# Optimization experiments

Hardware: AMD Instinct MI355X
Metric: run time of the kernel (lower is better)

Reference implementation:

```python
import jax, jax.numpy as jnp
import numpy as np

D_MODEL = 1024
NUM_HEADS = 16
HEAD_SIZE = D_MODEL // NUM_HEADS
THETA = 10000.0
MAX_SEQ_LEN = 4096


def _rope_tables():
    # (max_seq_len, head_size//2) cos/sin tables, matching RotaryPositionalEmbedding
    k = jnp.arange(HEAD_SIZE // 2, dtype=jnp.float32)
    inv_freq = 1.0 / (THETA ** (2.0 * k / HEAD_SIZE))
    pos = jnp.arange(MAX_SEQ_LEN, dtype=jnp.float32)
    ang = pos[:, None] * inv_freq[None, :]
    return jnp.cos(ang), jnp.sin(ang)


def _apply_rope(x, cos, sin):
    # x: (b, h, s, d); cos/sin: (s, d//2) -> broadcast over (b, h)
    x1 = x[..., ::2]
    x2 = x[..., 1::2]
    out_even = x1 * cos - x2 * sin
    out_odd = x2 * cos + x1 * sin
    # re-interleave pairs back to (..., d)
    return jnp.stack([out_even, out_odd], axis=-1).reshape(x.shape)


def setup_inputs() -> dict:
    key = jax.random.key(0)
    k1, k2, k3 = jax.random.split(key, 3)
    b, s = 1, 4096
    std_qkv = np.sqrt(2.0 / (D_MODEL + 3 * D_MODEL))
    std_o = np.sqrt(2.0 / (D_MODEL + D_MODEL))
    return {
        "x": jax.random.normal(k1, (b, s, D_MODEL), dtype=jnp.float32),
        "token_positions": jnp.arange(s, dtype=jnp.int32),
        "W_qkv": jax.random.normal(k2, (3 * D_MODEL, D_MODEL), dtype=jnp.float32) * std_qkv,
        "W_o": jax.random.normal(k3, (D_MODEL, D_MODEL), dtype=jnp.float32) * std_o,
    }


def reference(x, token_positions, W_qkv, W_o):
    b, s, _ = x.shape
    qkv = jnp.einsum("bsd,ed->bse", x, W_qkv)  # (b, s, 3*d_model)
    q, k, v = jnp.split(qkv, 3, axis=-1)

    def to_heads(t):
        return t.reshape(b, s, NUM_HEADS, HEAD_SIZE).transpose(0, 2, 1, 3)  # (b, h, s, hs)

    q, k, v = to_heads(q), to_heads(k), to_heads(v)

    cos_tab, sin_tab = _rope_tables()
    cos = cos_tab[token_positions]  # (s, hs//2)
    sin = sin_tab[token_positions]
    q = _apply_rope(q, cos, sin)
    k = _apply_rope(k, cos, sin)

    scale = 1.0 / jnp.sqrt(jnp.asarray(HEAD_SIZE, dtype=x.dtype))
    scores = jnp.einsum("bhqd,bhkd->bhqk", q, k) * scale  # (b, h, s, s)
    causal = jnp.tril(jnp.ones((s, s), dtype=bool))
    scores = jnp.where(causal, scores, jnp.finfo(scores.dtype).min)
    attn = jax.nn.softmax(scores, axis=-1)
    out = jnp.einsum("bhqk,bhkd->bhqd", attn, v)  # (b, h, s, hs)
    out = out.transpose(0, 2, 1, 3).reshape(b, s, D_MODEL)
    return jnp.einsum("bsd,ed->bse", out, W_o)
```

## Files before the change

### kernel.cpp

```cpp
#include <hip/hip_runtime.h>
#include <stdint.h>

typedef unsigned short u16;
typedef __attribute__((ext_vector_type(8))) short bf16x8;
typedef __attribute__((ext_vector_type(4))) float f32x4;

#define LN_THETA 9.210340371976184f
#define SLEN 4096
#define DMODEL 1024

__device__ __forceinline__ u16 f2bf(float f) {
  union { float f; unsigned u; } v; v.f = f;
  unsigned u = v.u;
  return (u16)((u + 0x7FFFu + ((u >> 16) & 1u)) >> 16);
}
__device__ __forceinline__ u16 f2bf_trunc(float f) {
  union { float f; unsigned u; } v; v.f = f;
  return (u16)(v.u >> 16);
}
__device__ __forceinline__ float bf2f(u16 b) {
  union { unsigned u; float f; } v; v.u = ((unsigned)b) << 16;
  return v.f;
}

__device__ __forceinline__ f32x4 mfma16(bf16x8 a, bf16x8 b, f32x4 c) {
  return __builtin_amdgcn_mfma_f32_16x16x32_bf16(a, b, c, 0, 0, 0);
}

__device__ __forceinline__ void async16(const u16* g, u16* l) {
  __builtin_amdgcn_global_load_lds(
      (const __attribute__((address_space(1))) unsigned int*)g,
      (__attribute__((address_space(3))) unsigned int*)l, 16, 0, 0);
}

__global__ void rope_tab_kernel(const int* __restrict__ tokpos,
                                float2* __restrict__ tab) {
  int t = blockIdx.x * 256 + threadIdx.x;
  int s = t >> 5, i = t & 31;
  float inv = expf(-(float)(2 * i) * (LN_THETA / 64.0f));
  float ang = (float)tokpos[s] * inv;
  float sn, cs;
  sincosf(ang, &sn, &cs);
  tab[t] = make_float2(cs, sn);
}

__global__ void cvt_all_kernel(const float* __restrict__ x,
                               const float* __restrict__ wqkv,
                               const float* __restrict__ wo,
                               u16* __restrict__ xb, u16* __restrict__ wqkvb,
                               u16* __restrict__ wob) {
  int i = blockIdx.x * 256 + threadIdx.x;
  const float* src;
  u16* dst;
  if (i < (1 << 20)) {
    src = x; dst = xb;
  } else if (i < (1 << 20) + (3 << 18)) {
    i -= (1 << 20); src = wqkv; dst = wqkvb;
  } else {
    i -= (1 << 20) + (3 << 18); src = wo; dst = wob;
  }
  float4 v = ((const float4*)src)[i];
  ushort4 o;
  o.x = f2bf(v.x); o.y = f2bf(v.y); o.z = f2bf(v.z); o.w = f2bf(v.w);
  ((ushort4*)dst)[i] = o;
}

__global__ __launch_bounds__(256) void gemm_qkv_kernel(
    const u16* __restrict__ A, const u16* __restrict__ B,
    u16* __restrict__ qb, u16* __restrict__ kb,
    u16* __restrict__ vbT, const float2* __restrict__ cstab) {
  const int K = 1024;
  __shared__ __align__(16) char smem[128 * 136 * 2];
  u16 (*As)[64] = (u16(*)[64])smem;
  u16 (*Bs)[64] = (u16(*)[64])(smem + 16384);
  u16 (*Ts)[136] = (u16(*)[136])smem;
  const int tid = threadIdx.x;
  const int wave = tid >> 6, lane = tid & 63;
  const int quad = lane >> 4, col = lane & 15;
  const int rowBase = blockIdx.x * 128;
  const int colBase = blockIdx.y * 128;
  const int wm = (wave >> 1) * 64, wn = (wave & 1) * 64;

  const int sr8 = lane >> 3;
  const int sseg = ((lane & 7) ^ sr8) * 8;
  const u16* gA = A + (size_t)(rowBase + wave * 8 + sr8) * K + sseg;
  const u16* gB = B + (size_t)(colBase + wave * 8 + sr8) * K + sseg;
  u16* ldsA = &As[wave * 8 + sr8][(lane & 7) * 8];
  u16* ldsB = &Bs[wave * 8 + sr8][(lane & 7) * 8];

  const int segh[2] = {((quad ^ (col & 7)) * 8), (((4 + quad) ^ (col & 7)) * 8)};

  f32x4 acc[4][4];
#pragma unroll
  for (int i = 0; i < 4; ++i)
#pragma unroll
    for (int j = 0; j < 4; ++j)
      acc[i][j] = f32x4{0.f, 0.f, 0.f, 0.f};

  for (int kk = 0; kk < K; kk += 64) {
    __syncthreads();
#pragma unroll
    for (int j = 0; j < 4; ++j) {
      async16(gA + (size_t)j * 32 * K + kk, ldsA + j * 32 * 64);
      async16(gB + (size_t)j * 32 * K + kk, ldsB + j * 32 * 64);
    }
    __syncthreads();
#pragma unroll
    for (int h = 0; h < 2; ++h) {
      bf16x8 af[4], bfr[4];
#pragma unroll
      for (int i = 0; i < 4; ++i)
        af[i] = *(const bf16x8*)&As[wm + i * 16 + col][segh[h]];
#pragma unroll
      for (int j = 0; j < 4; ++j)
        bfr[j] = *(const bf16x8*)&Bs[wn + j * 16 + col][segh[h]];
#pragma unroll
      for (int i = 0; i < 4; ++i)
#pragma unroll
        for (int j = 0; j < 4; ++j)
          acc[i][j] = mfma16(af[i], bfr[j], acc[i][j]);
    }
  }
  __syncthreads();

  const int sec = rowBase >> 10;

  if (sec < 2) {
    const float qs = (sec == 0) ? 0.125f : 1.0f;
#pragma unroll
    for (int j = 0; j < 4; ++j) {
      int sl = wn + j * 16 + col;
      int s = colBase + sl;
#pragma unroll
      for (int i = 0; i < 4; ++i) {
        int el = wm + i * 16 + quad * 4;
        int d = (rowBase + el) & 63;
        float v0 = acc[i][j][0], v1 = acc[i][j][1];
        float v2 = acc[i][j][2], v3 = acc[i][j][3];
        float2 cs0 = cstab[s * 32 + (d >> 1)];
        float2 cs1 = cstab[s * 32 + (d >> 1) + 1];
        ushort4 pk;
        pk.x = f2bf(qs * (v0 * cs0.x - v1 * cs0.y));
        pk.y = f2bf(qs * (v1 * cs0.x + v0 * cs0.y));
        pk.z = f2bf(qs * (v2 * cs1.x - v3 * cs1.y));
        pk.w = f2bf(qs * (v3 * cs1.x + v2 * cs1.y));
        *(ushort4*)&Ts[sl][el] = pk;
      }
    }
    __syncthreads();
    int sl = tid >> 1, hf = tid & 1;
    int hh = ((rowBase & 1023) >> 6) + hf;
    u16* dst = (sec == 0 ? qb : kb) + ((size_t)hh * SLEN + colBase + sl) * 64;
    const u16* srcp = &Ts[sl][hf * 64];
#pragma unroll
    for (int kq = 0; kq < 8; ++kq)
      ((int4*)dst)[kq] = ((const int4*)srcp)[kq];
  } else {
#pragma unroll
    for (int j = 0; j < 4; ++j) {
      int sl = wn + j * 16 + col;
#pragma unroll
      for (int i = 0; i < 4; ++i) {
        int el = wm + i * 16 + quad * 4;
#pragma unroll
        for (int r = 0; r < 4; ++r)
          Ts[el + r][sl] = f2bf(acc[i][j][r]);
      }
    }
    __syncthreads();
    int el = tid >> 1, sh = tid & 1;
    int e = rowBase - 2048 + el;
    int hh = e >> 6, d = e & 63;
    u16* dst = vbT + (size_t)(hh * 64 + d) * SLEN + colBase + sh * 64;
    const u16* srcp = &Ts[el][sh * 64];
#pragma unroll
    for (int kq = 0; kq < 8; ++kq)
      ((int4*)dst)[kq] = ((const int4*)srcp)[kq];
  }
}

__global__ __launch_bounds__(256) void gemm_out_kernel(
    const u16* __restrict__ A, const u16* __restrict__ B,
    float* __restrict__ outf) {
  const int K = 1024;
  __shared__ __align__(16) u16 As[128][64];
  __shared__ __align__(16) u16 Bs[64][64];
  const int tid = threadIdx.x;
  const int wave = tid >> 6, lane = tid & 63;
  const int quad = lane >> 4, col = lane & 15;
  const int rowBase = blockIdx.x * 128;
  const int colBase = blockIdx.y * 64;

  const int sr8 = lane >> 3;
  const int sseg = ((lane & 7) ^ sr8) * 8;
  const u16* gA = A + (size_t)(rowBase + wave * 8 + sr8) * K + sseg;
  const u16* gB = B + (size_t)(colBase + wave * 8 + sr8) * K + sseg;
  u16* ldsA = &As[wave * 8 + sr8][(lane & 7) * 8];
  u16* ldsB = &Bs[wave * 8 + sr8][(lane & 7) * 8];

  const int segh[2] = {((quad ^ (col & 7)) * 8), (((4 + quad) ^ (col & 7)) * 8)};

  f32x4 acc[2][4];
#pragma unroll
  for (int i = 0; i < 2; ++i)
#pragma unroll
    for (int j = 0; j < 4; ++j)
      acc[i][j] = f32x4{0.f, 0.f, 0.f, 0.f};

  for (int kk = 0; kk < K; kk += 64) {
    __syncthreads();
#pragma unroll
    for (int j = 0; j < 4; ++j)
      async16(gA + (size_t)j * 32 * K + kk, ldsA + j * 32 * 64);
#pragma unroll
    for (int j = 0; j < 2; ++j)
      async16(gB + (size_t)j * 32 * K + kk, ldsB + j * 32 * 64);
    __syncthreads();
#pragma unroll
    for (int h = 0; h < 2; ++h) {
      bf16x8 af[2], bfr[4];
#pragma unroll
      for (int i = 0; i < 2; ++i)
        af[i] = *(const bf16x8*)&As[wave * 32 + i * 16 + col][segh[h]];
#pragma unroll
      for (int j = 0; j < 4; ++j)
        bfr[j] = *(const bf16x8*)&Bs[j * 16 + col][segh[h]];
#pragma unroll
      for (int i = 0; i < 2; ++i)
#pragma unroll
        for (int j = 0; j < 4; ++j)
          acc[i][j] = mfma16(af[i], bfr[j], acc[i][j]);
    }
  }

#pragma unroll
  for (int i = 0; i < 2; ++i) {
    int r0 = rowBase + wave * 32 + i * 16 + quad * 4;
#pragma unroll
    for (int j = 0; j < 4; ++j) {
      int cc = colBase + j * 16 + col;
#pragma unroll
      for (int r = 0; r < 4; ++r)
        outf[(size_t)(r0 + r) * DMODEL + cc] = acc[i][j][r];
    }
  }
}

__global__ __launch_bounds__(128) void flash_kernel(
    const u16* __restrict__ qbuf, const u16* __restrict__ kbuf,
    const u16* __restrict__ vbT, u16* __restrict__ po,
    float* __restrict__ pl) {
  const int S = SLEN;
  const int h = blockIdx.x;
  const int y = blockIdx.y;
  int tile, c0, c1;
  if (y < 32) {
    tile = 32 + y; c0 = 0; c1 = 31;
  } else {
    int k = (y - 32) >> 1;
    if ((y - 32) & 1) { tile = 31 - k; c0 = 0; c1 = tile; }
    else { tile = 63 - k; c0 = 32; c1 = tile; }
  }
  const int id = (tile < 32) ? tile : (32 + 2 * (tile - 32) + (c0 ? 1 : 0));

  const int wave = threadIdx.x >> 6, lane = threadIdx.x & 63;
  const int quad = lane >> 4, col = lane & 15;
  const u16* Q = qbuf + (size_t)h * S * 64;
  const u16* Kh = kbuf + (size_t)h * S * 64;
  const u16* Vt = vbT + (size_t)h * 64 * S;

  __shared__ __align__(16) u16 Ks[64][64];
  __shared__ __align__(16) u16 Vs[64][64];
  __shared__ __align__(16) u16 Pld[2][2][16][72];

  const int sr = lane >> 3;
  const int sw = ((lane & 7) ^ sr) * 8;
  const int dcol = (lane & 7) * 8;
  const int segA = ((quad ^ (col & 7)) * 8);
  const int segB = (((quad ^ 4) ^ (col & 7)) * 8);

  const int qrow0 = tile * 64 + wave * 32;

  bf16x8 qf0[2], qf1[2];
#pragma unroll
  for (int i = 0; i < 2; ++i) {
    const u16* qp = &Q[(size_t)(qrow0 + i * 16 + col) * 64 + quad * 8];
    qf0[i] = *(const bf16x8*)qp;
    qf1[i] = *(const bf16x8*)(qp + 32);
  }

  const bf16x8 ones = {(short)0x3F80, (short)0x3F80, (short)0x3F80,
                       (short)0x3F80, (short)0x3F80, (short)0x3F80,
                       (short)0x3F80, (short)0x3F80};

  f32x4 o[2][4], lacc[2];
#pragma unroll
  for (int i = 0; i < 2; ++i) {
#pragma unroll
    for (int n = 0; n < 4; ++n) o[i][n] = f32x4{0.f, 0.f, 0.f, 0.f};
    lacc[i] = f32x4{0.f, 0.f, 0.f, 0.f};
  }

  for (int c = c0; c <= c1; ++c) {
    const int k0 = c * 64;
    __syncthreads();
    {
#pragma unroll
      for (int t = 0; t < 4; ++t) {
        int row = (t * 2 + wave) * 8 + sr;
        async16(Kh + (size_t)(k0 + row) * 64 + sw, &Ks[row][dcol]);
        async16(Vt + (size_t)row * S + k0 + sw, &Vs[row][dcol]);
      }
    }
    __syncthreads();

    bf16x8 kf0[4], kf1[4], vf0[4], vf1[4];
#pragma unroll
    for (int j = 0; j < 4; ++j) {
      kf0[j] = *(const bf16x8*)&Ks[16 * j + col][segA];
      kf1[j] = *(const bf16x8*)&Ks[16 * j + col][segB];
    }
#pragma unroll
    for (int n = 0; n < 4; ++n) {
      vf0[n] = *(const bf16x8*)&Vs[16 * n + col][segA];
      vf1[n] = *(const bf16x8*)&Vs[16 * n + col][segB];
    }
    const bool lastc = (c == tile);
#pragma unroll
    for (int i = 0; i < 2; ++i) {
      f32x4 s[4];
#pragma unroll
      for (int j = 0; j < 4; ++j)
        s[j] = mfma16(qf1[i], kf1[j],
                      mfma16(qf0[i], kf0[j], f32x4{0.f, 0.f, 0.f, 0.f}));
      float p[4][4];
#pragma unroll
      for (int r = 0; r < 4; ++r) {
        const int qrel = wave * 32 + i * 16 + quad * 4 + r;
#pragma unroll
        for (int j = 0; j < 4; ++j) {
          float e = __expf(s[j][r]);
          if (lastc && (16 * j + col > qrel)) e = 0.f;
          p[j][r] = e;
        }
      }
#pragma unroll
      for (int j = 0; j < 4; ++j)
#pragma unroll
        for (int r = 0; r < 4; ++r)
          Pld[wave][i][quad * 4 + r][16 * j + col] = f2bf_trunc(p[j][r]);
      bf16x8 pa0 = *(const bf16x8*)&Pld[wave][i][col][quad * 8];
      bf16x8 pa1 = *(const bf16x8*)&Pld[wave][i][col][quad * 8 + 32];
      lacc[i] = mfma16(pa1, ones, mfma16(pa0, ones, lacc[i]));
#pragma unroll
      for (int n = 0; n < 4; ++n)
        o[i][n] = mfma16(pa1, vf1[n], mfma16(pa0, vf0[n], o[i][n]));
    }
  }

  u16* pob = po + (((size_t)h * 96 + id) * 64) * 64;
  float* plb = pl + ((size_t)h * 96 + id) * 64;
#pragma unroll
  for (int i = 0; i < 2; ++i) {
#pragma unroll
    for (int r = 0; r < 4; ++r) {
      int rowl = wave * 32 + i * 16 + quad * 4 + r;
      u16* dst = pob + (size_t)rowl * 64 + col;
#pragma unroll
      for (int n = 0; n < 4; ++n) dst[16 * n] = f2bf(o[i][n][r]);
      if (col == 0) plb[rowl] = lacc[i][r];
    }
  }
}

__global__ __launch_bounds__(256) void reduce_kernel(
    const u16* __restrict__ po, const float* __restrict__ pl,
    u16* __restrict__ attn) {
  const int h = blockIdx.x, tile = blockIdx.y;
  const int tid = threadIdx.x;
  const int row = tid >> 2, dg = (tid & 3) * 16;
  int id0, ns;
  if (tile < 32) { id0 = tile; ns = 1; }
  else { id0 = 32 + 2 * (tile - 32); ns = 2; }

  float acc[16];
#pragma unroll
  for (int q = 0; q < 16; ++q) acc[q] = 0.f;
  float l = 0.f;
  for (int s = 0; s < ns; ++s) {
    const size_t base = ((size_t)h * 96 + id0 + s) * 64;
    const u16* p = po + (base + row) * 64 + dg;
    l += pl[base + row];
#pragma unroll
    for (int q = 0; q < 16; ++q) acc[q] += bf2f(p[q]);
  }
  float inv = 1.0f / l;
  u16* dst = attn + (size_t)(tile * 64 + row) * DMODEL + h * 64 + dg;
  ushort4 o0, o1, o2, o3;
  o0.x = f2bf(acc[0] * inv);  o0.y = f2bf(acc[1] * inv);
  o0.z = f2bf(acc[2] * inv);  o0.w = f2bf(acc[3] * inv);
  o1.x = f2bf(acc[4] * inv);  o1.y = f2bf(acc[5] * inv);
  o1.z = f2bf(acc[6] * inv);  o1.w = f2bf(acc[7] * inv);
  o2.x = f2bf(acc[8] * inv);  o2.y = f2bf(acc[9] * inv);
  o2.z = f2bf(acc[10] * inv); o2.w = f2bf(acc[11] * inv);
  o3.x = f2bf(acc[12] * inv); o3.y = f2bf(acc[13] * inv);
  o3.z = f2bf(acc[14] * inv); o3.w = f2bf(acc[15] * inv);
  ((ushort4*)dst)[0] = o0; ((ushort4*)dst)[1] = o1;
  ((ushort4*)dst)[2] = o2; ((ushort4*)dst)[3] = o3;
}

extern "C" void kernel_launch(void* const* d_in, const int* in_sizes, int n_in,
                              void* d_out, int out_size, void* d_ws,
                              size_t ws_size, hipStream_t stream) {
  const float* x = (const float*)d_in[0];
  const int* tokpos = (const int*)d_in[1];
  const float* wqkv = (const float*)d_in[2];
  const float* wo = (const float*)d_in[3];
  float* out = (float*)d_out;

  char* ws = (char*)d_ws;
  u16* xb    = (u16*)(ws);
  u16* wqkvb = (u16*)(ws + ((size_t)8 << 20));
  u16* wob   = (u16*)(ws + ((size_t)14 << 20));
  u16* qb    = (u16*)(ws + ((size_t)16 << 20));
  u16* kb    = (u16*)(ws + ((size_t)24 << 20));
  u16* vbT   = (u16*)(ws + ((size_t)32 << 20));
  u16* attn  = (u16*)(ws + ((size_t)40 << 20));
  float2* cstab = (float2*)(ws + ((size_t)48 << 20));
  u16* po    = (u16*)(ws);
  float* pl  = (float*)(ws + ((size_t)13 << 20));

  rope_tab_kernel<<<dim3(512), dim3(256), 0, stream>>>(tokpos, cstab);
  cvt_all_kernel<<<dim3(8192), dim3(256), 0, stream>>>(x, wqkv, wo, xb, wqkvb,
                                                       wob);
  gemm_qkv_kernel<<<dim3(24, 32), dim3(256), 0, stream>>>(
      wqkvb, xb, qb, kb, vbT, cstab);
  flash_kernel<<<dim3(16, 96), dim3(128), 0, stream>>>(qb, kb, vbT, po, pl);
  reduce_kernel<<<dim3(16, 64), dim3(256), 0, stream>>>(po, pl, attn);
  gemm_out_kernel<<<dim3(32, 16), dim3(256), 0, stream>>>(attn, wob, out);
}
```

Baseline: 220.2 us.

## Use four waves per flash block, fold log2e into Q, merge prep kernels

Restructures the flash attention kernel so each block runs four waves that each own 16 query rows, instead of two waves owning 32 rows each. This doubles the threads available per tile for latency hiding and splits the K/V load work more finely. The log2(e) factor is folded into the Q scale inside the QKV GEMM epilogue, so the softmax can use the hardware exp2 directly. The RoPE table and bf16 conversion kernels are merged into one launch to save a kernel launch. The cost is lower MFMA reuse of the K/V fragments per wave and more register and LDS footprint per block.

```diff
diff --git a/kernel.cpp b/kernel.cpp
--- a/kernel.cpp
+++ b/kernel.cpp
@@ -22,6 +22,13 @@
   union { unsigned u; float f; } v; v.u = ((unsigned)b) << 16;
   return v.f;
 }
+__device__ __forceinline__ float fexp2(float x) {
+#if __has_builtin(__builtin_amdgcn_exp2f)
+  return __builtin_amdgcn_exp2f(x);
+#else
+  return exp2f(x);
+#endif
+}
 
 __device__ __forceinline__ f32x4 mfma16(bf16x8 a, bf16x8 b, f32x4 c) {
   return __builtin_amdgcn_mfma_f32_16x16x32_bf16(a, b, c, 0, 0, 0);
@@ -33,23 +40,24 @@
       (__attribute__((address_space(3))) unsigned int*)l, 16, 0, 0);
 }
 
-__global__ void rope_tab_kernel(const int* __restrict__ tokpos,
-                                float2* __restrict__ tab) {
-  int t = blockIdx.x * 256 + threadIdx.x;
-  int s = t >> 5, i = t & 31;
-  float inv = expf(-(float)(2 * i) * (LN_THETA / 64.0f));
-  float ang = (float)tokpos[s] * inv;
-  float sn, cs;
-  sincosf(ang, &sn, &cs);
-  tab[t] = make_float2(cs, sn);
-}
-
-__global__ void cvt_all_kernel(const float* __restrict__ x,
-                               const float* __restrict__ wqkv,
-                               const float* __restrict__ wo,
-                               u16* __restrict__ xb, u16* __restrict__ wqkvb,
-                               u16* __restrict__ wob) {
-  int i = blockIdx.x * 256 + threadIdx.x;
+__global__ void prep_kernel(const int* __restrict__ tokpos,
+                            float2* __restrict__ tab,
+                            const float* __restrict__ x,
+                            const float* __restrict__ wqkv,
+                            const float* __restrict__ wo,
+                            u16* __restrict__ xb, u16* __restrict__ wqkvb,
+                            u16* __restrict__ wob) {
+  if (blockIdx.x < 512) {
+    int t = blockIdx.x * 256 + threadIdx.x;
+    int s = t >> 5, i = t & 31;
+    float inv = expf(-(float)(2 * i) * (LN_THETA / 64.0f));
+    float ang = (float)tokpos[s] * inv;
+    float sn, cs;
+    sincosf(ang, &sn, &cs);
+    tab[t] = make_float2(cs, sn);
+    return;
+  }
+  int i = (blockIdx.x - 512) * 256 + threadIdx.x;
   const float* src;
   u16* dst;
   if (i < (1 << 20)) {
@@ -126,7 +134,7 @@
   const int sec = rowBase >> 10;
 
   if (sec < 2) {
-    const float qs = (sec == 0) ? 0.125f : 1.0f;
+    const float qs = (sec == 0) ? 0.125f * 1.4426950408889634f : 1.0f;
 #pragma unroll
     for (int j = 0; j < 4; ++j) {
       int sl = wn + j * 16 + col;
@@ -246,7 +254,7 @@
   }
 }
 
-__global__ __launch_bounds__(128) void flash_kernel(
+__global__ __launch_bounds__(256) void flash_kernel(
     const u16* __restrict__ qbuf, const u16* __restrict__ kbuf,
     const u16* __restrict__ vbT, u16* __restrict__ po,
     float* __restrict__ pl) {
@@ -271,7 +279,7 @@
 
   __shared__ __align__(16) u16 Ks[64][64];
   __shared__ __align__(16) u16 Vs[64][64];
-  __shared__ __align__(16) u16 Pld[2][2][16][72];
+  __shared__ __align__(16) u16 Pld[4][16][72];
 
   const int sr = lane >> 3;
   const int sw = ((lane & 7) ^ sr) * 8;
@@ -279,35 +287,31 @@
   const int segA = ((quad ^ (col & 7)) * 8);
   const int segB = (((quad ^ 4) ^ (col & 7)) * 8);
 
-  const int qrow0 = tile * 64 + wave * 32;
-
-  bf16x8 qf0[2], qf1[2];
-#pragma unroll
-  for (int i = 0; i < 2; ++i) {
-    const u16* qp = &Q[(size_t)(qrow0 + i * 16 + col) * 64 + quad * 8];
-    qf0[i] = *(const bf16x8*)qp;
-    qf1[i] = *(const bf16x8*)(qp + 32);
+  const int qrow0 = tile * 64 + wave * 16;
+
+  bf16x8 qf0, qf1;
+  {
+    const u16* qp = &Q[(size_t)(qrow0 + col) * 64 + quad * 8];
+    qf0 = *(const bf16x8*)qp;
+    qf1 = *(const bf16x8*)(qp + 32);
   }
 
   const bf16x8 ones = {(short)0x3F80, (short)0x3F80, (short)0x3F80,
                        (short)0x3F80, (short)0x3F80, (short)0x3F80,
                        (short)0x3F80, (short)0x3F80};
 
-  f32x4 o[2][4], lacc[2];
-#pragma unroll
-  for (int i = 0; i < 2; ++i) {
-#pragma unroll
-    for (int n = 0; n < 4; ++n) o[i][n] = f32x4{0.f, 0.f, 0.f, 0.f};
-    lacc[i] = f32x4{0.f, 0.f, 0.f, 0.f};
-  }
+  f32x4 o[4], lacc;
+#pragma unroll
+  for (int n = 0; n < 4; ++n) o[n] = f32x4{0.f, 0.f, 0.f, 0.f};
+  lacc = f32x4{0.f, 0.f, 0.f, 0.f};
 
   for (int c = c0; c <= c1; ++c) {
     const int k0 = c * 64;
     __syncthreads();
     {
 #pragma unroll
-      for (int t = 0; t < 4; ++t) {
-        int row = (t * 2 + wave) * 8 + sr;
+      for (int t = 0; t < 2; ++t) {
+        int row = wave * 16 + t * 8 + sr;
         async16(Kh + (size_t)(k0 + row) * 64 + sw, &Ks[row][dcol]);
         async16(Vt + (size_t)row * S + k0 + sw, &Vs[row][dcol]);
       }
@@ -326,50 +330,44 @@
       vf1[n] = *(const bf16x8*)&Vs[16 * n + col][segB];
     }
     const bool lastc = (c == tile);
-#pragma unroll
-    for (int i = 0; i < 2; ++i) {
-      f32x4 s[4];
-#pragma unroll
-      for (int j = 0; j < 4; ++j)
-        s[j] = mfma16(qf1[i], kf1[j],
-                      mfma16(qf0[i], kf0[j], f32x4{0.f, 0.f, 0.f, 0.f}));
-      float p[4][4];
-#pragma unroll
-      for (int r = 0; r < 4; ++r) {
-        const int qrel = wave * 32 + i * 16 + quad * 4 + r;
-#pragma unroll
-        for (int j = 0; j < 4; ++j) {
-          float e = __expf(s[j][r]);
-          if (lastc && (16 * j + col > qrel)) e = 0.f;
-          p[j][r] = e;
-        }
+    f32x4 s[4];
+#pragma unroll
+    for (int j = 0; j < 4; ++j)
+      s[j] = mfma16(qf1, kf1[j],
+                    mfma16(qf0, kf0[j], f32x4{0.f, 0.f, 0.f, 0.f}));
+    float p[4][4];
+#pragma unroll
+    for (int r = 0; r < 4; ++r) {
+      const int qabs = qrow0 + quad * 4 + r;
+#pragma unroll
+      for (int j = 0; j < 4; ++j) {
+        float e = fexp2(s[j][r]);
+        if (lastc && (k0 + 16 * j + col > qabs)) e = 0.f;
+        p[j][r] = e;
       }
-#pragma unroll
-      for (int j = 0; j < 4; ++j)
-#pragma unroll
-        for (int r = 0; r < 4; ++r)
-          Pld[wave][i][quad * 4 + r][16 * j + col] = f2bf_trunc(p[j][r]);
-      bf16x8 pa0 = *(const bf16x8*)&Pld[wave][i][col][quad * 8];
-      bf16x8 pa1 = *(const bf16x8*)&Pld[wave][i][col][quad * 8 + 32];
-      lacc[i] = mfma16(pa1, ones, mfma16(pa0, ones, lacc[i]));
-#pragma unroll
-      for (int n = 0; n < 4; ++n)
-        o[i][n] = mfma16(pa1, vf1[n], mfma16(pa0, vf0[n], o[i][n]));
-    }
+    }
+#pragma unroll
+    for (int j = 0; j < 4; ++j)
+#pragma unroll
+      for (int r = 0; r < 4; ++r)
+        Pld[wave][quad * 4 + r][16 * j + col] = f2bf_trunc(p[j][r]);
+    bf16x8 pa0 = *(const bf16x8*)&Pld[wave][col][quad * 8];
+    bf16x8 pa1 = *(const bf16x8*)&Pld[wave][col][quad * 8 + 32];
+    lacc = mfma16(pa1, ones, mfma16(pa0, ones, lacc));
+#pragma unroll
+    for (int n = 0; n < 4; ++n)
+      o[n] = mfma16(pa1, vf1[n], mfma16(pa0, vf0[n], o[n]));
   }
 
   u16* pob = po + (((size_t)h * 96 + id) * 64) * 64;
   float* plb = pl + ((size_t)h * 96 + id) * 64;
 #pragma unroll
-  for (int i = 0; i < 2; ++i) {
-#pragma unroll
-    for (int r = 0; r < 4; ++r) {
-      int rowl = wave * 32 + i * 16 + quad * 4 + r;
-      u16* dst = pob + (size_t)rowl * 64 + col;
-#pragma unroll
-      for (int n = 0; n < 4; ++n) dst[16 * n] = f2bf(o[i][n][r]);
-      if (col == 0) plb[rowl] = lacc[i][r];
-    }
+  for (int r = 0; r < 4; ++r) {
+    int rowl = wave * 16 + quad * 4 + r;
+    u16* dst = pob + (size_t)rowl * 64 + col;
+#pragma unroll
+    for (int n = 0; n < 4; ++n) dst[16 * n] = f2bf(o[n][r]);
+    if (col == 0) plb[rowl] = lacc[r];
   }
 }
 
@@ -430,12 +428,11 @@
   u16* po    = (u16*)(ws);
   float* pl  = (float*)(ws + ((size_t)13 << 20));
 
-  rope_tab_kernel<<<dim3(512), dim3(256), 0, stream>>>(tokpos, cstab);
-  cvt_all_kernel<<<dim3(8192), dim3(256), 0, stream>>>(x, wqkv, wo, xb, wqkvb,
-                                                       wob);
+  prep_kernel<<<dim3(8704), dim3(256), 0, stream>>>(tokpos, cstab, x, wqkv, wo,
+                                                    xb, wqkvb, wob);
   gemm_qkv_kernel<<<dim3(24, 32), dim3(256), 0, stream>>>(
       wqkvb, xb, qb, kb, vbT, cstab);
-  flash_kernel<<<dim3(16, 96), dim3(128), 0, stream>>>(qb, kb, vbT, po, pl);
+  flash_kernel<<<dim3(16, 96), dim3(256), 0, stream>>>(qb, kb, vbT, po, pl);
   reduce_kernel<<<dim3(16, 64), dim3(256), 0, stream>>>(po, pl, attn);
   gemm_out_kernel<<<dim3(32, 16), dim3(256), 0, stream>>>(attn, wob, out);
 }
```

Measured after the change: 210.4 us. -4.4%, faster.
